# Kernel tuning notes

Hardware: AMD Instinct MI355X
Metric: run time of the kernel (lower is better)

## Reference

```python
import jax, jax.numpy as jnp
import numpy as np

RES_X, RES_Y = 256, 256          # resolution_px
RES_X_MM, RES_Y_MM = 32.0, 32.0  # resolution_mm
FOCAL_MM = 35.0
N_MODELS, N_TRI = 8, 1000
BATCH = 2
EPS = 1e-8


def _calibration_matrix():
    fx = FOCAL_MM * RES_X / RES_X_MM
    fy = FOCAL_MM * RES_Y / RES_Y_MM
    return np.array([[fx, 0.0, RES_X / 2.0],
                     [0.0, fy, RES_Y / 2.0],
                     [0.0, 0.0, 1.0]], dtype=np.float32)


def _pixel_grid():
    # matches np.mgrid[0:res_x, 0:res_y] -> concat(xx, yy) -> reshape(-1, 2)
    xx, yy = np.mgrid[0:RES_X, 0:RES_Y]
    grid = np.concatenate((xx[..., None], yy[..., None]), axis=-1)
    return jnp.asarray(grid.reshape(-1, 2).astype(np.float32))  # (P, 2)


def setup_inputs() -> dict:
    key = jax.random.key(0)
    k1, k2, k3 = jax.random.split(key, 3)
    meshes = jax.random.normal(k1, (N_MODELS, N_TRI, 3, 3), dtype=jnp.float32)
    base = jnp.concatenate(
        [jnp.eye(3, dtype=jnp.float32), jnp.array([[0.0], [0.0], [5.0]], jnp.float32)], axis=1)
    camera_poses = base[None] + 0.05 * jax.random.normal(k2, (BATCH, 3, 4), dtype=jnp.float32)
    model_idxs = jax.random.randint(k3, (BATCH,), 0, N_MODELS)
    return {"meshes": meshes, "K": jnp.asarray(_calibration_matrix()),
            "model_idxs": model_idxs, "camera_poses": camera_poses}


def _rasterize_one(mesh, cam, K, grid):
    # mesh: (T,3,3), cam: (3,4), grid: (P,2)
    T = mesh.shape[0]
    pts = mesh.reshape(-1, 3)                                   # (3T, 3)
    hom = jnp.concatenate([pts, jnp.ones((pts.shape[0], 1), pts.dtype)], axis=-1)
    proj = K @ cam @ hom.T                                      # (3, 3T)
    xy = (proj[:2] / (proj[2:3] + EPS)).T                       # (3T, 2)
    tri = xy.reshape(T, 3, 2)

    e0 = tri[:, 1] - tri[:, 0]
    e1 = tri[:, 2] - tri[:, 1]
    e2 = tri[:, 0] - tri[:, 2]
    N = (e0[:, 0] * e2[:, 1] - e0[:, 1] * e2[:, 0] + EPS)[:, None]  # (T,1)

    px, py = grid[:, 0][None], grid[:, 1][None]                 # (1,P) each

    def edge_term(e, v):
        # (e cross (v - p)) * N, computed without materializing (T,P,2)
        return (e[:, 0:1] * (v[:, 1:2] - py) - e[:, 1:2] * (v[:, 0:1] - px)) * N

    t1 = jnp.maximum(edge_term(e0, tri[:, 0]), 0.0)
    t2 = jnp.maximum(edge_term(e1, tri[:, 1]), 0.0)
    t3 = jnp.maximum(edge_term(e2, tri[:, 2]), 0.0)
    score = t1 * t2 * t3                                        # (T, P)

    mn = jnp.min(score, axis=1, keepdims=True)
    mx = jnp.max(score, axis=1, keepdims=True)
    norm = jnp.tanh((score - mn) / (mx - mn + EPS))
    return jnp.sum(norm, axis=0).reshape(RES_Y, RES_X)


def reference(meshes, K, model_idxs, camera_poses):
    grid = _pixel_grid()
    return jax.vmap(lambda i, cam: _rasterize_one(meshes[i], cam, K, grid))(
        model_idxs, camera_poses)
```

## Files before the change

kernel.cpp:

```cpp
#include <hip/hip_runtime.h>

#define RES    256
#define NPIX   (RES * RES)
#define NTRI   1000
#define EPSF   1e-8f
#define CPT    12
#define NCHK   4
#define TPC    250
#define LOG2E2 2.8853900817779268f


__global__ __launch_bounds__(256) void tri_setup(
    const float* __restrict__ meshes, const float* __restrict__ Km,
    const int* __restrict__ midx, const float* __restrict__ cams,
    float* __restrict__ coef, unsigned int* __restrict__ bbox,
    float* __restrict__ out, int nout)
{
    const int blk = blockIdx.x;
    const int b = blk / NTRI;
    const int t = blk - b * NTRI;

    { const int g = blk * 256 + threadIdx.x; if (g < nout) out[g] = 0.0f; }

    const float* cam = cams + b * 12;
    float M[12];
#pragma unroll
    for (int i = 0; i < 3; ++i) {
        const float k0 = Km[i*3+0], k1 = Km[i*3+1], k2 = Km[i*3+2];
#pragma unroll
        for (int j = 0; j < 4; ++j)
            M[i*4+j] = k0*cam[j] + k1*cam[4+j] + k2*cam[8+j];
    }
    const int m = midx[b];
    const float* tv = meshes + ((size_t)m * NTRI + t) * 9;
    float vx[3], vy[3];
#pragma unroll
    for (int v = 0; v < 3; ++v) {
        const float X = tv[v*3+0], Y = tv[v*3+1], Z = tv[v*3+2];
        const float w = M[8]*X + M[9]*Y + M[10]*Z + M[11] + EPSF;
        vx[v] = (M[0]*X + M[1]*Y + M[2]*Z + M[3]) / w;
        vy[v] = (M[4]*X + M[5]*Y + M[6]*Z + M[7]) / w;
    }

    const float e0x = vx[1]-vx[0], e0y = vy[1]-vy[0];
    const float e1x = vx[2]-vx[1], e1y = vy[2]-vy[1];
    const float e2x = vx[0]-vx[2], e2y = vy[0]-vy[2];
    const float N = e0x*e2y - e0y*e2x + EPSF;

    const float a0 = N*e0y, b0 = -N*e0x, c0 = N*(e0x*vy[0] - e0y*vx[0]);
    const float a1 = N*e1y, b1 = -N*e1x, c1 = N*(e1x*vy[1] - e1y*vx[1]);
    const float a2 = N*e2y, b2 = -N*e2x, c2 = N*(e2x*vy[2] - e2y*vx[2]);

    float mnx = fminf(fminf(vx[0],vx[1]),vx[2]);
    float mxx = fmaxf(fmaxf(vx[0],vx[1]),vx[2]);
    float mny = fminf(fminf(vy[0],vy[1]),vy[2]);
    float mxy = fmaxf(fmaxf(vy[0],vy[1]),vy[2]);
    mnx = fmaxf(fminf(mnx, 1e6f), -1e6f);  mxx = fmaxf(fminf(mxx, 1e6f), -1e6f);
    mny = fmaxf(fminf(mny, 1e6f), -1e6f);  mxy = fmaxf(fminf(mxy, 1e6f), -1e6f);
    const int bx0 = max(0,     (int)floorf(mnx) - 1);
    const int bx1 = min(RES-1, (int)ceilf (mxx) + 1);
    const int by0 = max(0,     (int)floorf(mny) - 1);
    const int by1 = min(RES-1, (int)ceilf (mxy) + 1);
    const bool empty = (bx0 > bx1) || (by0 > by1);

    float rowmax = 0.0f;
    if (!empty && threadIdx.x <= (unsigned)(by1 - by0)) {
        const float fy = (float)(by0 + (int)threadIdx.x);
        const float B0 = fmaf(b0, fy, c0);
        const float B1 = fmaf(b1, fy, c1);
        const float B2 = fmaf(b2, fy, c2);

        const float l0 = 1.0f / (fabsf(a0) + fabsf(B0) + 1e-30f);
        const float l1 = 1.0f / (fabsf(a1) + fabsf(B1) + 1e-30f);
        const float l2 = 1.0f / (fabsf(a2) + fabsf(B2) + 1e-30f);
        const float n0 = a0*l0, p0 = B0*l0;
        const float n1 = a1*l1, p1 = B1*l1;
        const float n2 = a2*l2, p2 = B2*l2;
        const float qa = 3.0f * n0*n1*n2;
        const float qb = 2.0f * (n0*n1*p2 + n0*n2*p1 + n1*n2*p0);
        const float qc = n0*p1*p2 + n1*p0*p2 + n2*p0*p1;

        float x1, x2;
        if (fabsf(qa) > 1e-30f) {
            const float disc = qb*qb - 4.0f*qa*qc;
            if (disc >= 0.0f) {
                const float rt = sqrtf(disc);
                x1 = (-qb - rt) / (2.0f*qa);
                x2 = (-qb + rt) / (2.0f*qa);
            } else {
                x1 = x2 = -qb / (2.0f*qa);
            }
        } else if (fabsf(qb) > 1e-30f) {
            x1 = x2 = -qc / qb;
        } else {
            x1 = x2 = (float)bx0;
        }

        const int f1 = (int)floorf(x1), f2 = (int)floorf(x2);
        int cand[12] = { f1-1, f1, f1+1, f1+2,  f2-1, f2, f2+1, f2+2,
                         bx0, bx0+1, bx1-1, bx1 };
#pragma unroll
        for (int k = 0; k < 12; ++k) {
            const int xi = min(max(cand[k], bx0), bx1);
            const float fx = (float)xi;
            const float u1 = fmaxf(fmaf(a0, fx, B0), 0.0f);
            const float u2 = fmaxf(fmaf(a1, fx, B1), 0.0f);
            const float u3 = fmaxf(fmaf(a2, fx, B2), 0.0f);
            rowmax = fmaxf(rowmax, u1*u2*u3);
        }
    }

#pragma unroll
    for (int off = 32; off > 0; off >>= 1)
        rowmax = fmaxf(rowmax, __shfl_down(rowmax, off, 64));
    __shared__ float smx[4];
    __shared__ float scorner[4];
    const int lane = threadIdx.x & 63, wv = threadIdx.x >> 6;
    if (lane == 0) smx[wv] = rowmax;

    if (threadIdx.x < 4) {
        const float fx = (threadIdx.x & 1) ? 255.0f : 0.0f;
        const float fy = (threadIdx.x & 2) ? 255.0f : 0.0f;
        const float u1 = fmaxf(fmaf(a0, fx, fmaf(b0, fy, c0)), 0.0f);
        const float u2 = fmaxf(fmaf(a1, fx, fmaf(b1, fy, c1)), 0.0f);
        const float u3 = fmaxf(fmaf(a2, fx, fmaf(b2, fy, c2)), 0.0f);
        scorner[threadIdx.x] = u1*u2*u3;
    }
    __syncthreads();

    if (threadIdx.x == 0) {
        const float mn = fminf(fminf(scorner[0], scorner[1]),
                               fminf(scorner[2], scorner[3]));
        float mx = fmaxf(fmaxf(smx[0], smx[1]), fmaxf(smx[2], smx[3]));
        mx = fmaxf(mx, mn);
        const float ik = LOG2E2 / (mx - mn + EPSF);
        float* r = coef + ((size_t)b * NTRI + t) * CPT;
        r[0]=a0; r[1]=b0; r[2]=c0; r[3]=a1; r[4]=b1; r[5]=c1;
        r[6]=a2; r[7]=b2; r[8]=c2;
        r[9]=ik; r[10]=mn*ik; r[11]=0.0f;
        bbox[(size_t)b * NTRI + t] = empty ? 0x00FF00FFu
            : ((unsigned)bx0 | ((unsigned)bx1 << 8) |
               ((unsigned)by0 << 16) | ((unsigned)by1 << 24));
    }
}

__global__ __launch_bounds__(256) void rasterize(
    const float* __restrict__ coef, const unsigned int* __restrict__ bbox,
    float* __restrict__ out)
{
    __shared__ float cl[TPC * CPT];
    __shared__ unsigned short s_list[256];
    __shared__ int s_n, wbase[4];

    const int blk   = blockIdx.x;
    const int b     = blk >> 10;
    const int rest  = blk & 1023;
    const int chunk = rest & (NCHK - 1);
    const int tile  = rest >> 2;
    const int tx0   = (tile >> 4) << 4;
    const int ty0   = (tile & 15) << 4;

    const int l  = threadIdx.x & 63;
    const int wv = threadIdx.x >> 6;

    if (threadIdx.x == 0) s_n = 0;
    __syncthreads();

    const int base = chunk * TPC;
    const int t = threadIdx.x;
    bool hit = false;
    if (t < TPC) {
        const unsigned int w = bbox[(size_t)b * NTRI + base + t];
        const int tbx0 = w & 255, tbx1 = (w >> 8) & 255;
        const int tby0 = (w >> 16) & 255, tby1 = w >> 24;
        hit = !(tbx1 < tx0 || tbx0 > tx0 + 15 || tby1 < ty0 || tby0 > ty0 + 15);
    }
    const unsigned long long m = __ballot(hit);
    if (l == 0) wbase[wv] = atomicAdd(&s_n, (int)__popcll(m));
    __syncthreads();
    if (hit) {
        const int pos = wbase[wv] + (int)__popcll(m & ((1ull << l) - 1ull));
        s_list[pos] = (unsigned short)t;
    }
    __syncthreads();
    const int n = s_n;

    {
        const float* cb = coef + ((size_t)b * NTRI + base) * CPT;
        for (int j = threadIdx.x; j < n * CPT; j += 256) {
            const int k = j / CPT, w = j - k * CPT;
            cl[j] = cb[(int)s_list[k] * CPT + w];
        }
    }
    __syncthreads();

    const int px = tx0 + (threadIdx.x >> 4);
    const int py = ty0 + (threadIdx.x & 15);
    const float fx = (float)px, fy = (float)py;

    float acc = 0.0f;
#pragma unroll 2
    for (int k = 0; k < n; ++k) {
        const float* r = &cl[k * CPT];
        const float u1 = fmaxf(fmaf(r[0], fx, fmaf(r[1], fy, r[2])), 0.0f);
        const float u2 = fmaxf(fmaf(r[3], fx, fmaf(r[4], fy, r[5])), 0.0f);
        const float u3 = fmaxf(fmaf(r[6], fx, fmaf(r[7], fy, r[8])), 0.0f);
        const float e  = __builtin_amdgcn_exp2f(fmaf(u1*u2*u3, r[9], -r[10]));
        acc += __builtin_amdgcn_rcpf(1.0f + e);
    }

    const float v = fmaf(-2.0f, acc, (float)n);
    atomicAdd(out + (size_t)b * NPIX + (size_t)px * RES + py, v);
}

extern "C" void kernel_launch(void* const* d_in, const int* in_sizes, int n_in,
                              void* d_out, int out_size, void* d_ws, size_t ws_size,
                              hipStream_t stream)
{
    const float* meshes = (const float*)d_in[0];
    const float* Km     = (const float*)d_in[1];
    const int*   midx   = (const int*)d_in[2];
    const float* cams   = (const float*)d_in[3];
    float* out = (float*)d_out;

    const int batch = in_sizes[3] / 12;

    float* coef = (float*)d_ws;
    unsigned int* bbox =
        (unsigned int*)((char*)d_ws + (size_t)batch * NTRI * CPT * sizeof(float));

    tri_setup<<<dim3(batch * NTRI), dim3(256), 0, stream>>>(
        meshes, Km, midx, cams, coef, bbox, out, batch * NPIX);
    rasterize<<<dim3(batch * 256 * NCHK), dim3(256), 0, stream>>>(coef, bbox, out);
}
```

Measured before the change: 90.93 us.

## Process all triangles per tile in one block, drop atomics and zero-init

Each rasterize block now handles all 1000 triangles for its 16x16 tile, binning them in four ballot passes and streaming the hit list through shared memory in batches of 320. Because one block owns each tile, the output is written directly, which removes the global atomicAdd and the zeroing of the output in tri_setup. The cost is a quarter as many blocks (512), so parallelism drops and latency hiding may suffer, and batches add extra syncs for tiles with many triangles.

```diff
diff --git a/kernel.cpp b/kernel.cpp
--- a/kernel.cpp
+++ b/kernel.cpp
@@ -5,22 +5,18 @@
 #define NTRI   1000
 #define EPSF   1e-8f
 #define CPT    12
-#define NCHK   4
-#define TPC    250
+#define CAPC   320
 #define LOG2E2 2.8853900817779268f
 
 
 __global__ __launch_bounds__(256) void tri_setup(
     const float* __restrict__ meshes, const float* __restrict__ Km,
     const int* __restrict__ midx, const float* __restrict__ cams,
-    float* __restrict__ coef, unsigned int* __restrict__ bbox,
-    float* __restrict__ out, int nout)
+    float* __restrict__ coef, unsigned int* __restrict__ bbox)
 {
     const int blk = blockIdx.x;
     const int b = blk / NTRI;
     const int t = blk - b * NTRI;
-
-    { const int g = blk * 256 + threadIdx.x; if (g < nout) out[g] = 0.0f; }
 
     const float* cam = cams + b * 12;
     float M[12];
@@ -148,69 +144,71 @@
     const float* __restrict__ coef, const unsigned int* __restrict__ bbox,
     float* __restrict__ out)
 {
-    __shared__ float cl[TPC * CPT];
-    __shared__ unsigned short s_list[256];
-    __shared__ int s_n, wbase[4];
-
-    const int blk   = blockIdx.x;
-    const int b     = blk >> 10;
-    const int rest  = blk & 1023;
-    const int chunk = rest & (NCHK - 1);
-    const int tile  = rest >> 2;
-    const int tx0   = (tile >> 4) << 4;
-    const int ty0   = (tile & 15) << 4;
+    __shared__ float cl[CAPC * CPT];
+    __shared__ unsigned short s_list[1024];
+    __shared__ int s_n;
+
+    const int blk  = blockIdx.x;
+    const int b    = blk >> 8;
+    const int tile = blk & 255;
+    const int tx0  = (tile >> 4) << 4;
+    const int ty0  = (tile & 15) << 4;
 
     const int l  = threadIdx.x & 63;
-    const int wv = threadIdx.x >> 6;
-
-    if (threadIdx.x == 0) s_n = 0;
+    const int tid = threadIdx.x;
+
+    if (tid == 0) s_n = 0;
     __syncthreads();
 
-    const int base = chunk * TPC;
-    const int t = threadIdx.x;
-    bool hit = false;
-    if (t < TPC) {
-        const unsigned int w = bbox[(size_t)b * NTRI + base + t];
-        const int tbx0 = w & 255, tbx1 = (w >> 8) & 255;
-        const int tby0 = (w >> 16) & 255, tby1 = w >> 24;
-        hit = !(tbx1 < tx0 || tbx0 > tx0 + 15 || tby1 < ty0 || tby0 > ty0 + 15);
-    }
-    const unsigned long long m = __ballot(hit);
-    if (l == 0) wbase[wv] = atomicAdd(&s_n, (int)__popcll(m));
-    __syncthreads();
-    if (hit) {
-        const int pos = wbase[wv] + (int)__popcll(m & ((1ull << l) - 1ull));
-        s_list[pos] = (unsigned short)t;
+    const unsigned int* bbp = bbox + (size_t)b * NTRI;
+#pragma unroll
+    for (int g = 0; g < 4; ++g) {
+        const int idx = g * 250 + tid;
+        bool hit = false;
+        if (tid < 250) {
+            const unsigned int w = bbp[idx];
+            const int tbx0 = w & 255, tbx1 = (w >> 8) & 255;
+            const int tby0 = (w >> 16) & 255, tby1 = w >> 24;
+            hit = !(tbx1 < tx0 || tbx0 > tx0 + 15 || tby1 < ty0 || tby0 > ty0 + 15);
+        }
+        const unsigned long long m = __ballot(hit);
+        int base = 0;
+        if (l == 0) base = atomicAdd(&s_n, (int)__popcll(m));
+        base = __builtin_amdgcn_readfirstlane(base);
+        if (hit) {
+            const int pos = base + (int)__popcll(m & ((1ull << l) - 1ull));
+            s_list[pos] = (unsigned short)idx;
+        }
     }
     __syncthreads();
     const int n = s_n;
 
-    {
-        const float* cb = coef + ((size_t)b * NTRI + base) * CPT;
-        for (int j = threadIdx.x; j < n * CPT; j += 256) {
+    const int px = tx0 + (tid >> 4);
+    const int py = ty0 + (tid & 15);
+    const float fx = (float)px, fy = (float)py;
+    const float* cb = coef + (size_t)b * NTRI * CPT;
+
+    float acc = 0.0f;
+    for (int start = 0; start < n; start += CAPC) {
+        const int cnt = min(CAPC, n - start);
+        for (int j = tid; j < cnt * CPT; j += 256) {
             const int k = j / CPT, w = j - k * CPT;
-            cl[j] = cb[(int)s_list[k] * CPT + w];
-        }
-    }
-    __syncthreads();
-
-    const int px = tx0 + (threadIdx.x >> 4);
-    const int py = ty0 + (threadIdx.x & 15);
-    const float fx = (float)px, fy = (float)py;
-
-    float acc = 0.0f;
+            cl[j] = cb[(int)s_list[start + k] * CPT + w];
+        }
+        __syncthreads();
 #pragma unroll 2
-    for (int k = 0; k < n; ++k) {
-        const float* r = &cl[k * CPT];
-        const float u1 = fmaxf(fmaf(r[0], fx, fmaf(r[1], fy, r[2])), 0.0f);
-        const float u2 = fmaxf(fmaf(r[3], fx, fmaf(r[4], fy, r[5])), 0.0f);
-        const float u3 = fmaxf(fmaf(r[6], fx, fmaf(r[7], fy, r[8])), 0.0f);
-        const float e  = __builtin_amdgcn_exp2f(fmaf(u1*u2*u3, r[9], -r[10]));
-        acc += __builtin_amdgcn_rcpf(1.0f + e);
-    }
-
-    const float v = fmaf(-2.0f, acc, (float)n);
-    atomicAdd(out + (size_t)b * NPIX + (size_t)px * RES + py, v);
+        for (int k = 0; k < cnt; ++k) {
+            const float* r = &cl[k * CPT];
+            const float u1 = fmaxf(fmaf(r[0], fx, fmaf(r[1], fy, r[2])), 0.0f);
+            const float u2 = fmaxf(fmaf(r[3], fx, fmaf(r[4], fy, r[5])), 0.0f);
+            const float u3 = fmaxf(fmaf(r[6], fx, fmaf(r[7], fy, r[8])), 0.0f);
+            const float e  = __builtin_amdgcn_exp2f(fmaf(u1*u2*u3, r[9], -r[10]));
+            acc += __builtin_amdgcn_rcpf(1.0f + e);
+        }
+        __syncthreads();
+    }
+
+    out[(size_t)b * NPIX + (size_t)px * RES + py] = fmaf(-2.0f, acc, (float)n);
 }
 
 extern "C" void kernel_launch(void* const* d_in, const int* in_sizes, int n_in,
@@ -230,6 +228,6 @@
         (unsigned int*)((char*)d_ws + (size_t)batch * NTRI * CPT * sizeof(float));
 
     tri_setup<<<dim3(batch * NTRI), dim3(256), 0, stream>>>(
-        meshes, Km, midx, cams, coef, bbox, out, batch * NPIX);
-    rasterize<<<dim3(batch * 256 * NCHK), dim3(256), 0, stream>>>(coef, bbox, out);
+        meshes, Km, midx, cams, coef, bbox);
+    rasterize<<<dim3(batch * 256), dim3(256), 0, stream>>>(coef, bbox, out);
 }
```

Measured after the change: 119.2 us. 31.0% more time.
